# Performance work log

Measured on AMD Instinct MI355X. Metric: run time of the kernel, lower is better.

## Reference

```python
import jax, jax.numpy as jnp
import numpy as np

S, FEAT, D, H, L, DFF, C = 1024, 64, 512, 8, 2, 2048, 10
DB = D // 4  # distance-bias MLP hidden
NFREQ = D // 6  # 85 -> 6*85=510 dims, padded to 512
EPS = 1e-5


def _layernorm(x, g, b):
    mu = jnp.mean(x, axis=-1, keepdims=True)
    var = jnp.mean(jnp.square(x - mu), axis=-1, keepdims=True)
    return (x - mu) * jax.lax.rsqrt(var + EPS) * g + b


def setup_inputs() -> dict:
    key = jax.random.key(0)
    ks = iter(jax.random.split(key, 40))
    def w(shape, scale=0.02):
        return (jax.random.normal(next(ks), shape, jnp.float32) * scale)
    inp = {
        'features': jax.random.normal(next(ks), (S, FEAT), jnp.float32),
        'positions': jax.random.uniform(next(ks), (S, 3), jnp.float32),
        'freq_bands': jnp.asarray(10.0 ** np.linspace(0.0, 10.0, NFREQ), jnp.float32),
        'in_w': w((FEAT, D)), 'in_b': jnp.zeros((D,), jnp.float32),
        'qw': w((L, D, D)), 'qb': jnp.zeros((L, D), jnp.float32),
        'kw': w((L, D, D)), 'kb': jnp.zeros((L, D), jnp.float32),
        'vw': w((L, D, D)), 'vb': jnp.zeros((L, D), jnp.float32),
        'ow': w((L, D, D)), 'ob': jnp.zeros((L, D), jnp.float32),
        'db1w': w((L, 1, DB), 0.5), 'db1b': jnp.zeros((L, DB), jnp.float32),
        'db2w': w((L, DB, H), 0.1), 'db2b': jnp.zeros((L, H), jnp.float32),
        'n1g': jnp.ones((L, D), jnp.float32), 'n1b': jnp.zeros((L, D), jnp.float32),
        'n2g': jnp.ones((L, D), jnp.float32), 'n2b': jnp.zeros((L, D), jnp.float32),
        'f1w': w((L, D, DFF)), 'f1b': jnp.zeros((L, DFF), jnp.float32),
        'f2w': w((L, DFF, D)), 'f2b': jnp.zeros((L, D), jnp.float32),
        'c1w': w((D, D // 2)), 'c1b': jnp.zeros((D // 2,), jnp.float32),
        'c2w': w((D // 2, C)), 'c2b': jnp.zeros((C,), jnp.float32),
    }
    return inp


def _forward(features, positions, freq_bands, in_w, in_b, qw, qb, kw, kb, vw, vb,
             ow, ob, db1w, db1b, db2w, db2b, n1g, n1b, n2g, n2b,
             f1w, f1b, f2w, f2b, c1w, c1b, c2w, c2b):
    d_model = in_w.shape[1]
    nhead = db2w.shape[-1]
    head_dim = d_model // nhead
    scale = 1.0 / np.sqrt(head_dim)

    x = features[None] @ in_w + in_b            # [1, S, D]
    pos = positions[None]                        # [1, S, 3]

    # 3D sinusoidal positional encoding: [sin0,cos0,sin1,cos1,sin2,cos2]
    enc = []
    for i in range(3):
        cs = pos[..., i:i + 1] * freq_bands      # [1, S, NFREQ] (broadcast)
        enc.append(jnp.sin(cs))
        enc.append(jnp.cos(cs))
    pe = jnp.concatenate(enc, axis=-1)           # [1, S, 6*NFREQ]
    if pe.shape[-1] > d_model:
        pe = pe[..., :d_model]
    elif pe.shape[-1] < d_model:
        pe = jnp.pad(pe, ((0, 0), (0, 0), (0, d_model - pe.shape[-1])))
    x = x + pe

    # pairwise distances [1, S, S, 1]; safe sqrt (zero grad on diagonal)
    diff = pos[:, :, None, :] - pos[:, None, :, :]
    sq = jnp.sum(jnp.square(diff), axis=-1, keepdims=True)
    dist = jnp.sqrt(jnp.where(sq > 0, sq, 1.0)) * (sq > 0)

    n_layers = qw.shape[0]
    seq = x.shape[1]
    for l in range(n_layers):
        q = (x @ qw[l] + qb[l]).reshape(1, seq, nhead, head_dim)
        k = (x @ kw[l] + kb[l]).reshape(1, seq, nhead, head_dim)
        v = (x @ vw[l] + vb[l]).reshape(1, seq, nhead, head_dim)
        scores = jnp.einsum('bihd,bjhd->bhij', q, k) * scale  # [1,H,S,S]
        hbias = jax.nn.relu(dist @ db1w[l] + db1b[l])          # [1,S,S,DB]
        bias = jnp.einsum('bijc,ch->bhij', hbias, db2w[l]) + db2b[l][None, :, None, None]
        attn = jax.nn.softmax(scores + bias, axis=-1)
        out = jnp.einsum('bhij,bjhd->bihd', attn, v).reshape(1, seq, d_model)
        out = out @ ow[l] + ob[l]
        x = _layernorm(x + out, n1g[l], n1b[l])
        ffn = jax.nn.relu(x @ f1w[l] + f1b[l]) @ f2w[l] + f2b[l]
        x = _layernorm(x + ffn, n2g[l], n2b[l])

    pooled = jnp.mean(x, axis=1)                 # [1, D]
    return jax.nn.relu(pooled @ c1w + c1b) @ c2w + c2b  # [1, C]


def reference(features, positions, freq_bands, in_w, in_b, qw, qb, kw, kb, vw, vb,
              ow, ob, db1w, db1b, db2w, db2b, n1g, n1b, n2g, n2b,
              f1w, f1b, f2w, f2b, c1w, c1b, c2w, c2b):
    return _forward(features, positions, freq_bands, in_w, in_b, qw, qb, kw, kb, vw, vb,
                    ow, ob, db1w, db1b, db2w, db2b, n1g, n1b, n2g, n2b,
                    f1w, f1b, f2w, f2b, c1w, c1b, c2w, c2b)
```

## Files before the change

### kernel.cpp

```cpp
#include <hip/hip_runtime.h>

namespace {
constexpr int kS   = 1024;
constexpr int kD   = 512;
constexpr int kDFF = 2048;
constexpr int kNF  = 85;
}

typedef __attribute__((ext_vector_type(8))) short bhalf8_t;
typedef _Float16 half8_t __attribute__((ext_vector_type(8)));
typedef __attribute__((ext_vector_type(4))) float f32x4_t;

__device__ __forceinline__ float wave_sum(float v) {
#pragma unroll
    for (int o = 1; o < 64; o <<= 1) v += __shfl_xor(v, o, 64);
    return v;
}
__device__ __forceinline__ unsigned short f2h(float f) {
    _Float16 h = (_Float16)f;
    return __builtin_bit_cast(unsigned short, h);
}
__device__ __forceinline__ float h2f(unsigned short u) {
    return (float)__builtin_bit_cast(_Float16, u);
}

__global__ __launch_bounds__(256)
void prep_a_k(const float* __restrict__ feat, const float* __restrict__ pos,
              const float* __restrict__ fb, const float* __restrict__ in_w,
              const float* __restrict__ in_b, float* __restrict__ x,
              unsigned short* __restrict__ xb,
              float* __restrict__ dist,
              const float* __restrict__ a_, const float* __restrict__ b_,
              float* __restrict__ bp_out)
{
    __shared__ float smem[128];
    int bid = blockIdx.x;
    int t = threadIdx.x;
    if (bid < 1024) {
        int s = bid;
        if (t < 64) smem[t] = feat[s * 64 + t];
        __syncthreads();
        float acc0 = in_b[t], acc1 = in_b[t + 256];
#pragma unroll 8
        for (int c = 0; c < 64; ++c) {
            float fv = smem[c];
            acc0 = fmaf(fv, in_w[c * kD + t], acc0);
            acc1 = fmaf(fv, in_w[c * kD + 256 + t], acc1);
        }
        float pe0 = 0.f, pe1 = 0.f;
        {
            int d = t;
            if (d < 6 * kNF) {
                int seg = d / kNF, idx = d - seg * kNF;
                float cs = pos[s * 3 + (seg >> 1)] * fb[idx];
                pe0 = (seg & 1) ? cosf(cs) : sinf(cs);
            }
            d = t + 256;
            if (d < 6 * kNF) {
                int seg = d / kNF, idx = d - seg * kNF;
                float cs = pos[s * 3 + (seg >> 1)] * fb[idx];
                pe1 = (seg & 1) ? cosf(cs) : sinf(cs);
            }
        }
        float o0 = acc0 + pe0, o1 = acc1 + pe1;
        x[s * kD + t]        = o0;
        x[s * kD + 256 + t]  = o1;
        xb[s * kD + t]       = f2h(o0);
        xb[s * kD + 256 + t] = f2h(o1);
    } else if (bid < 2048) {
        int i = bid - 1024;
        float px = pos[i * 3], py = pos[i * 3 + 1], pz = pos[i * 3 + 2];
        for (int j = t; j < kS; j += 256) {
            float dx = px - pos[j * 3], dy = py - pos[j * 3 + 1], dz = pz - pos[j * 3 + 2];
            float sq = dx * dx + dy * dy + dz * dz;
            dist[(long)i * kS + j] = sq > 0.f ? sqrtf(sq) : 0.f;
        }
    } else {
        int l = bid - 2048;
        const float* ap = a_ + l * 128;
        const float* bp = b_ + l * 128;
        float* out = bp_out + l * 128;
        if (t < 128) {
            float a = ap[t], b = bp[t];
            smem[t] = (a != 0.f) ? (-b / a) : 3.0e38f;
        }
        __syncthreads();
        for (int ksz = 2; ksz <= 128; ksz <<= 1) {
            for (int j = ksz >> 1; j > 0; j >>= 1) {
                if (t < 128) {
                    int ixj = t ^ j;
                    if (ixj > t) {
                        bool up = ((t & ksz) == 0);
                        float x0 = smem[t], x1 = smem[ixj];
                        if ((x0 > x1) == up) { smem[t] = x1; smem[ixj] = x0; }
                    }
                }
                __syncthreads();
            }
        }
        if (t < 128) out[t] = smem[t];
    }
}

__device__ __forceinline__ void tr_tile32(const float* __restrict__ in,
                                          unsigned short* __restrict__ out,
                                          int N, int K, int k0, int n0, int t,
                                          float* tile )
{
    int r = t >> 3, c4 = (t & 7) * 4;
    float4 v = *reinterpret_cast<const float4*>(&in[(long)(k0 + r) * N + n0 + c4]);
    tile[r * 33 + c4] = v.x; tile[r * 33 + c4 + 1] = v.y;
    tile[r * 33 + c4 + 2] = v.z; tile[r * 33 + c4 + 3] = v.w;
    __syncthreads();
    int nr = t >> 3, kq = (t & 7) * 4;
    unsigned short h[4];
#pragma unroll
    for (int j = 0; j < 4; ++j) h[j] = f2h(tile[(kq + j) * 33 + nr]);
    *reinterpret_cast<ushort4*>(&out[(long)(n0 + nr) * K + k0 + kq]) =
        make_ushort4(h[0], h[1], h[2], h[3]);
}

__global__ __launch_bounds__(256)
void prep_w_k(const float* __restrict__ qw, const float* __restrict__ kw,
              const float* __restrict__ vw, const float* __restrict__ ow,
              unsigned short* __restrict__ qwb, unsigned short* __restrict__ kwb,
              unsigned short* __restrict__ vwb, unsigned short* __restrict__ owb,
              const float* __restrict__ f1w, unsigned short* __restrict__ f1wb,
              const float* __restrict__ f2w, unsigned short* __restrict__ f2wb,
              const float* __restrict__ a_, const float* __restrict__ b_,
              const float* __restrict__ w2, const float* __restrict__ b2,
              const float* __restrict__ bp, float* __restrict__ Atab,
              float* __restrict__ Btab)
{
    __shared__ float smem[32 * 33];
    int bid = blockIdx.x;
    int t = threadIdx.x;
    if (bid < 2048) {
        int zz = bid >> 8, rem = bid & 255;
        int mat = zz >> 1, layer = zz & 1;
        const float* in = (mat == 0) ? qw : (mat == 1) ? kw : (mat == 2) ? vw : ow;
        unsigned short* out = (mat == 0) ? qwb : (mat == 1) ? kwb : (mat == 2) ? vwb : owb;
        tr_tile32(in + (long)layer * 262144, out + (long)layer * 262144,
                  512, 512, (rem & 15) * 32, (rem >> 4) * 32, t, smem);
    } else if (bid < 4096) {
        int l = bid - 2048;
        int z = l >> 10;
        tr_tile32(f1w + (long)z * 1048576, f1wb + (long)z * 1048576,
                  2048, 512, (l & 15) * 32, ((l >> 4) & 63) * 32, t, smem);
    } else if (bid < 6144) {
        int l = bid - 4096;
        int z = l >> 10;
        tr_tile32(f2w + (long)z * 1048576, f2wb + (long)z * 1048576,
                  512, 2048, (l & 63) * 32, ((l >> 6) & 15) * 32, t, smem);
    } else {
        int l = bid - 6144;
        int seg = l % 129, ly = l / 129;
        const float* ap = a_ + ly * 128;
        const float* bpp = b_ + ly * 128;
        const float* w2p = w2 + ly * 1024;
        const float* b2p = b2 + ly * 8;
        const float* bpl = bp + ly * 128;
        float* At = Atab + ly * 1040;
        float* Bt = Btab + ly * 1040;

        float m;
        if (seg == 0)        m = bpl[0] - 1.0f;
        else if (seg == 128) m = bpl[127] + 1.0f;
        else                 m = 0.5f * (bpl[seg - 1] + bpl[seg]);

        int h = t & 7, cg = t >> 3;
        float A = 0.f, B = 0.f;
#pragma unroll
        for (int j = 0; j < 4; ++j) {
            int c = cg * 4 + j;
            float a = ap[c], b = bpp[c];
            if (fmaf(a, m, b) > 0.f) {
                float w = w2p[c * 8 + h];
                A = fmaf(a, w, A);
                B = fmaf(b, w, B);
            }
        }
#pragma unroll
        for (int off = 8; off < 64; off <<= 1) {
            A += __shfl_xor(A, off, 64);
            B += __shfl_xor(B, off, 64);
        }
        int w = t >> 6, lane = t & 63;
        if (lane < 8) { smem[w * 8 + lane] = A; smem[32 + w * 8 + lane] = B; }
        __syncthreads();
        if (t < 8) {
            float At_ = smem[t] + smem[8 + t] + smem[16 + t] + smem[24 + t];
            float Bt_ = smem[32 + t] + smem[40 + t] + smem[48 + t] + smem[56 + t];
            At[seg * 8 + t] = At_;
            Bt[seg * 8 + t] = Bt_ + b2p[t];
        }
    }
}

constexpr int BKp = 72;
constexpr int ASZ = 64 * BKp;
constexpr int BSZ = 128 * BKp;

template<int K>
__device__ __forceinline__ void gemm_core(
    const unsigned short* __restrict__ Ap, const unsigned short* __restrict__ Bp,
    int lda, int ldb, int bm, int bn, int tid,
    unsigned short* __restrict__ As, unsigned short* __restrict__ Bs,
    f32x4_t acc[2][4])
{
    int w = tid >> 6, lane = tid & 63, quad = lane >> 4, l16 = lane & 15;
    int wm = (w >> 1) * 32, wn = (w & 1) * 64;
    int ar = tid >> 2, ac = (tid & 3) * 16;
    int br = tid >> 1, bc = (tid & 1) * 32;
    const unsigned short* pa = Ap + (long)(bm + ar) * lda + ac;
    const unsigned short* pb = Bp + (long)(bn + br) * ldb + bc;

    bhalf8_t a0_0, a0_1, b0_0, b0_1, b0_2, b0_3;
    bhalf8_t a1_0, a1_1, b1_0, b1_1, b1_2, b1_3;

#define LDG(S, k0) do { \
    a##S##_0 = *reinterpret_cast<const bhalf8_t*>(pa + (k0)); \
    a##S##_1 = *reinterpret_cast<const bhalf8_t*>(pa + (k0) + 8); \
    b##S##_0 = *reinterpret_cast<const bhalf8_t*>(pb + (k0)); \
    b##S##_1 = *reinterpret_cast<const bhalf8_t*>(pb + (k0) + 8); \
    b##S##_2 = *reinterpret_cast<const bhalf8_t*>(pb + (k0) + 16); \
    b##S##_3 = *reinterpret_cast<const bhalf8_t*>(pb + (k0) + 24); } while (0)
#define STG(S, as, bs) do { \
    *reinterpret_cast<bhalf8_t*>(&(as)[ar * BKp + ac])      = a##S##_0; \
    *reinterpret_cast<bhalf8_t*>(&(as)[ar * BKp + ac + 8])  = a##S##_1; \
    *reinterpret_cast<bhalf8_t*>(&(bs)[br * BKp + bc])      = b##S##_0; \
    *reinterpret_cast<bhalf8_t*>(&(bs)[br * BKp + bc + 8])  = b##S##_1; \
    *reinterpret_cast<bhalf8_t*>(&(bs)[br * BKp + bc + 16]) = b##S##_2; \
    *reinterpret_cast<bhalf8_t*>(&(bs)[br * BKp + bc + 24]) = b##S##_3; } while (0)

    constexpr int NT = K / 64;
    LDG(0, 0);
    STG(0, As, Bs);
    if (NT > 1) LDG(1, 64);
#pragma unroll
    for (int t = 0; t < NT; ++t) {
        __syncthreads();
        if (t + 2 < NT) {
            if ((t & 1) == 0) LDG(0, (t + 2) * 64);
            else              LDG(1, (t + 2) * 64);
        }
        const unsigned short* as = As + (t & 1) * ASZ;
        const unsigned short* bs = Bs + (t & 1) * BSZ;
#pragma unroll
        for (int kq = 0; kq < 2; ++kq) {
            bhalf8_t af[2], bf[4];
#pragma unroll
            for (int i = 0; i < 2; ++i)
                af[i] = *reinterpret_cast<const bhalf8_t*>(
                    &as[(wm + i * 16 + l16) * BKp + kq * 32 + quad * 8]);
#pragma unroll
            for (int j = 0; j < 4; ++j)
                bf[j] = *reinterpret_cast<const bhalf8_t*>(
                    &bs[(wn + j * 16 + l16) * BKp + kq * 32 + quad * 8]);
#pragma unroll
            for (int i = 0; i < 2; ++i)
#pragma unroll
                for (int j = 0; j < 4; ++j)
                    acc[i][j] = __builtin_amdgcn_mfma_f32_16x16x32_f16(
                        __builtin_bit_cast(half8_t, af[i]), __builtin_bit_cast(half8_t, bf[j]),
                        acc[i][j], 0, 0, 0);
        }
        if (t + 1 < NT) {
            if (((t + 1) & 1) == 0) STG(0, As, Bs);
            else                    STG(1, As + ASZ, Bs + BSZ);
        }
    }
#undef LDG
#undef STG
}

__global__ __launch_bounds__(256, 2)
void qkv_bias_k(const unsigned short* __restrict__ xb,
                const unsigned short* __restrict__ qwb, const unsigned short* __restrict__ kwb,
                const unsigned short* __restrict__ vwb,
                const float* __restrict__ qbias, const float* __restrict__ kbias,
                const float* __restrict__ vbias,
                unsigned short* __restrict__ qb2, unsigned short* __restrict__ kb2,
                unsigned short* __restrict__ vtb,
                const float* __restrict__ dist, const float* __restrict__ bp,
                const float* __restrict__ Atab, const float* __restrict__ Btab,
                unsigned short* __restrict__ bmap, unsigned int* __restrict__ cnt)
{
    __shared__ __align__(16) unsigned short smem[2 * ASZ + 2 * BSZ];
    int bid = blockIdx.x;
    int tid = threadIdx.x;
    if (bid < 192) {
        int z = bid >> 6, rem = bid & 63;
        int bm = (rem & 15) * 64, bn = (rem >> 4) * 128;
        const unsigned short* Bp = (z == 1) ? kwb : (z == 2) ? vwb : qwb;
        const float* bias = (z == 1) ? kbias : (z == 2) ? vbias : qbias;
        f32x4_t acc[2][4] = {};
        gemm_core<512>(xb, Bp, 512, 512, bm, bn, tid, smem, smem + 2 * ASZ, acc);

        int w = tid >> 6, lane = tid & 63, quad = lane >> 4, l16 = lane & 15;
        int wm = (w >> 1) * 32, wn = (w & 1) * 64;
        if (z == 2) {
            __syncthreads();
            unsigned short* T = smem;
#pragma unroll
            for (int j = 0; j < 4; ++j) {
                int ln = wn + j * 16 + l16;
                float bv = bias[bn + ln];
#pragma unroll
                for (int i = 0; i < 2; ++i)
#pragma unroll
                    for (int r = 0; r < 4; ++r)
                        T[ln * BKp + wm + i * 16 + quad * 4 + r] =
                            f2h((acc[i][j][r] + bv) * 1024.f);
            }
            __syncthreads();
            int nr = tid >> 1, mc = (tid & 1) * 32;
            int gn = bn + nr;
            unsigned short* dst = vtb + (long)(gn >> 6) * 65536
                                + (long)(gn & 63) * 1024 + bm + mc;
#pragma unroll
            for (int jj = 0; jj < 4; ++jj)
                *reinterpret_cast<bhalf8_t*>(dst + jj * 8) =
                    *reinterpret_cast<const bhalf8_t*>(&T[nr * BKp + mc + jj * 8]);
        } else {
#pragma unroll
            for (int j = 0; j < 4; ++j) {
                int n = bn + wn + j * 16 + l16;
                float bv = bias[n];
                unsigned short* dst = ((z == 1) ? kb2 : qb2)
                    + (long)(n >> 6) * 131072 + (n & 63);
#pragma unroll
                for (int i = 0; i < 2; ++i)
#pragma unroll
                    for (int r = 0; r < 4; ++r) {
                        int m = bm + wm + i * 16 + quad * 4 + r;
                        float s = acc[i][j][r] + bv;
                        unsigned short hi = f2h(s);
                        dst[(long)m * 128]      = hi;
                        dst[(long)m * 128 + 64] = (z == 0) ? f2h(s - h2f(hi)) : hi;
                    }
            }
        }
    } else {
        if (bid == 192 && tid < 8) cnt[tid] = 0;
        float* fs = reinterpret_cast<float*>(smem);
        float* bps = fs;
        float* Ah  = fs + 128;
        float* Bh  = fs + 1160;
        int t = tid;
        if (t < 128) bps[t] = bp[t];
        for (int i = t; i < 1032; i += 256) { Ah[i] = Atab[i]; Bh[i] = Btab[i]; }
        __syncthreads();
        long i = ((long)(bid - 192) * 256 + t) * 4;
        float4 d4 = *reinterpret_cast<const float4*>(dist + i);
        float dv[4] = {d4.x, d4.y, d4.z, d4.w};
        int seg[4];
#pragma unroll
        for (int j = 0; j < 4; ++j) {
            float tv = dv[j];
            int lo = 0, hi = 128;
            while (lo < hi) { int mid = (lo + hi) >> 1; if (bps[mid] < tv) lo = mid + 1; else hi = mid; }
            seg[j] = lo;
        }
        long gm  = i >> 10;
        int gn0  = (int)(i & 1023);
        int zz   = gn0 >> 7, nb = (gn0 >> 4) & 7, c4 = gn0 & 15;
        long pbase = gm * 1024 + zz * 128 + nb;
#pragma unroll
        for (int h = 0; h < 8; ++h) {
            unsigned short* bh = bmap + (long)h * 1048576 + pbase;
#pragma unroll
            for (int j = 0; j < 4; ++j)
                bh[(c4 + j) * 8] =
                    f2h(fmaf(Ah[seg[j] * 8 + h], dv[j], Bh[seg[j] * 8 + h]));
        }
    }
}

__global__ __launch_bounds__(256, 2)
void bgemm_ffn1_k(const unsigned short* __restrict__ A,
                  const unsigned short* __restrict__ B,
                  const float* __restrict__ bias,
                  unsigned short* __restrict__ hb)
{
    __shared__ __align__(16) unsigned short smem[2 * ASZ + 2 * BSZ];
    int tid = threadIdx.x;
    int bm = blockIdx.x * 64, bn = blockIdx.y * 128;
    f32x4_t acc[2][4] = {};
    gemm_core<512>(A, B, 512, 512, bm, bn, tid, smem, smem + 2 * ASZ, acc);

    int w = tid >> 6, lane = tid & 63, quad = lane >> 4, l16 = lane & 15;
    int wm = (w >> 1) * 32, wn = (w & 1) * 64;
#pragma unroll
    for (int j = 0; j < 4; ++j) {
        int n = bn + wn + j * 16 + l16;
        float bv = bias[n];
#pragma unroll
        for (int i = 0; i < 2; ++i)
#pragma unroll
            for (int r = 0; r < 4; ++r) {
                int m = bm + wm + i * 16 + quad * 4 + r;
                hb[(long)m * kDFF + n] = f2h(fmaxf(acc[i][j][r] + bv, 0.f));
            }
    }
}

template<int K>
__global__ __launch_bounds__(256, 2)
void bgemm_k(const unsigned short* __restrict__ A, const unsigned short* __restrict__ B,
             int N, int lda, int ldb, unsigned short* __restrict__ Cpart)
{
    __shared__ __align__(16) unsigned short smem[2 * ASZ + 2 * BSZ];
    int tid = threadIdx.x;
    int ks = blockIdx.z;
    const unsigned short* Ap = A + (long)ks * K;
    const unsigned short* Bp = B + (long)ks * K;
    int bm = blockIdx.x * 64, bn = blockIdx.y * 128;
    f32x4_t acc[2][4] = {};
    gemm_core<K>(Ap, Bp, lda, ldb, bm, bn, tid, smem, smem + 2 * ASZ, acc);

    int w = tid >> 6, lane = tid & 63, quad = lane >> 4, l16 = lane & 15;
    int wm = (w >> 1) * 32, wn = (w & 1) * 64;
    unsigned short* Cp = Cpart + (long)ks * kS * N;
#pragma unroll
    for (int i = 0; i < 2; ++i)
#pragma unroll
        for (int j = 0; j < 4; ++j)
#pragma unroll
            for (int r = 0; r < 4; ++r) {
                int m = bm + wm + i * 16 + quad * 4 + r;
                int n = bn + wn + j * 16 + l16;
                Cp[(long)m * N + n] = f2h(acc[i][j][r]);
            }
}

__global__ __launch_bounds__(256, 3)
void flash_part_k(const unsigned short* __restrict__ qb2, const unsigned short* __restrict__ kb2,
                  const unsigned short* __restrict__ vtb, const unsigned short* __restrict__ bmap,
                  unsigned short* __restrict__ po, float* __restrict__ pm, float* __restrict__ pl)
{
    constexpr int KP = 136;
    __shared__ __align__(16) unsigned short Klds[128 * KP];
    __shared__ __align__(16) unsigned short Vlds[64 * KP];

    int tid = threadIdx.x;
    int w    = tid >> 6;
    int lane = tid & 63;
    int quad = lane >> 4, l16 = lane & 15;

    int wg  = blockIdx.x;
    int lin = (wg & 7) * 128 + (wg >> 3);
    int qbg = lin & 15;
    int h   = (lin >> 4) & 7;
    int z   = lin >> 7;
    int qb  = qbg * 4 + w;
    int bm  = qb * 16;
    int k0  = z * 128;

    const unsigned short* Qh = qb2 + (long)h * 131072;
    const unsigned short* Kh = kb2 + (long)h * 131072;
    const unsigned short* Vh = vtb + (long)h * 65536;
    const unsigned short* Bm = bmap + (long)h * 1048576;

    {
        int kr = tid >> 1, kc = (tid & 1) * 64;
#pragma unroll
        for (int j = 0; j < 8; ++j)
            *reinterpret_cast<bhalf8_t*>(&Klds[kr * KP + kc + j * 8]) =
                *reinterpret_cast<const bhalf8_t*>(&Kh[(long)(k0 + kr) * 128 + kc + j * 8]);
        int vr = tid >> 2, vc = (tid & 3) * 32;
#pragma unroll
        for (int j = 0; j < 4; ++j)
            *reinterpret_cast<bhalf8_t*>(&Vlds[vr * KP + vc + j * 8]) =
                *reinterpret_cast<const bhalf8_t*>(&Vh[(long)vr * 1024 + k0 + vc + j * 8]);
    }

    bhalf8_t aq[4];
#pragma unroll
    for (int kq = 0; kq < 4; ++kq)
        aq[kq] = *reinterpret_cast<const bhalf8_t*>(
            &Qh[(long)(bm + l16) * 128 + kq * 32 + quad * 8]);
    bhalf8_t bias8[4];
#pragma unroll
    for (int r = 0; r < 4; ++r) {
        int gm = bm + quad * 4 + r;
        bias8[r] = *reinterpret_cast<const bhalf8_t*>(
            &Bm[(long)gm * 1024 + z * 128 + l16 * 8]);
    }

    __syncthreads();

    f32x4_t sacc[8] = {};
#pragma unroll
    for (int kq = 0; kq < 4; ++kq) {
        bhalf8_t bk[8];
#pragma unroll
        for (int nb = 0; nb < 8; ++nb)
            bk[nb] = *reinterpret_cast<const bhalf8_t*>(
                &Klds[(nb * 16 + l16) * KP + kq * 32 + quad * 8]);
#pragma unroll
        for (int nb = 0; nb < 8; ++nb)
            sacc[nb] = __builtin_amdgcn_mfma_f32_16x16x32_f16(
                __builtin_bit_cast(half8_t, aq[kq]), __builtin_bit_cast(half8_t, bk[nb]),
                sacc[nb], 0, 0, 0);
    }

    float m_r[4] = {-3.0e38f, -3.0e38f, -3.0e38f, -3.0e38f};
#pragma unroll
    for (int nb = 0; nb < 8; ++nb)
#pragma unroll
        for (int r = 0; r < 4; ++r) {
            float bias = h2f((unsigned short)bias8[r][nb]);
            float s = fmaf(sacc[nb][r], 0.125f, bias);
            sacc[nb][r] = s;
            m_r[r] = fmaxf(m_r[r], s);
        }
#pragma unroll
    for (int r = 0; r < 4; ++r) {
        float m_ = m_r[r];
#pragma unroll
        for (int off = 1; off < 16; off <<= 1) m_ = fmaxf(m_, __shfl_xor(m_, off, 64));
        m_r[r] = m_;
    }

    __syncthreads();

    unsigned short* Ps = Klds + w * 16 * KP;
    float l_r[4];
#pragma unroll
    for (int r = 0; r < 4; ++r) {
        int row = quad * 4 + r;
        float mN = m_r[r];
        float s_ = 0.f;
#pragma unroll
        for (int nb = 0; nb < 8; ++nb) {
            float p = __expf(sacc[nb][r] - mN);
            Ps[row * KP + nb * 16 + l16] = f2h(p * 16384.f);
            s_ += p;
        }
#pragma unroll
        for (int off = 1; off < 16; off <<= 1) s_ += __shfl_xor(s_, off, 64);
        l_r[r] = s_;
    }

    long sbase = (((long)z * 8 + h) * 64 + qb) * 16;
    if (l16 == 0) {
#pragma unroll
        for (int r = 0; r < 4; ++r) {
            pm[sbase + quad * 4 + r] = m_r[r];
            pl[sbase + quad * 4 + r] = l_r[r];
        }
    }

    f32x4_t oacc[4] = {};
#pragma unroll
    for (int kq2 = 0; kq2 < 4; ++kq2) {
        bhalf8_t ap = *reinterpret_cast<const bhalf8_t*>(&Ps[l16 * KP + kq2 * 32 + quad * 8]);
#pragma unroll
        for (int j2 = 0; j2 < 4; ++j2) {
            bhalf8_t bv = *reinterpret_cast<const bhalf8_t*>(
                &Vlds[(j2 * 16 + l16) * KP + kq2 * 32 + quad * 8]);
            oacc[j2] = __builtin_amdgcn_mfma_f32_16x16x32_f16(
                __builtin_bit_cast(half8_t, ap), __builtin_bit_cast(half8_t, bv),
                oacc[j2], 0, 0, 0);
        }
    }

    unsigned short* pob = po + sbase * 64;
#pragma unroll
    for (int j2 = 0; j2 < 4; ++j2)
#pragma unroll
        for (int r = 0; r < 4; ++r)
            pob[(quad * 4 + r) * 64 + j2 * 16 + l16] =
                f2h(oacc[j2][r] * (1.f / 16777216.f));
}

__global__ __launch_bounds__(256)
void flash_merge_k(const unsigned short* __restrict__ po, const float* __restrict__ pm,
                   const float* __restrict__ pl, unsigned short* __restrict__ aob)
{
    int t = blockIdx.x * 256 + threadIdx.x;
    int c8  = t & 7;
    int row = (t >> 3) & 15;
    int qb  = (t >> 7) & 63;
    int h   = t >> 13;
    long sidx = (((long)h * 64) + qb) * 16 + row;

    float m[8];
    float M = -3.0e38f;
#pragma unroll
    for (int z = 0; z < 8; ++z) { m[z] = pm[z * 8192 + sidx]; M = fmaxf(M, m[z]); }
    float w[8], lt = 0.f;
#pragma unroll
    for (int z = 0; z < 8; ++z) {
        w[z] = __expf(m[z] - M);
        lt = fmaf(pl[z * 8192 + sidx], w[z], lt);
    }
    float acc[8] = {};
#pragma unroll
    for (int z = 0; z < 8; ++z) {
        const unsigned short* p = po + (z * 8192 + sidx) * 64 + c8 * 8;
        ushort4 a = *reinterpret_cast<const ushort4*>(p);
        ushort4 b = *reinterpret_cast<const ushort4*>(p + 4);
        acc[0] = fmaf(h2f(a.x), w[z], acc[0]); acc[1] = fmaf(h2f(a.y), w[z], acc[1]);
        acc[2] = fmaf(h2f(a.z), w[z], acc[2]); acc[3] = fmaf(h2f(a.w), w[z], acc[3]);
        acc[4] = fmaf(h2f(b.x), w[z], acc[4]); acc[5] = fmaf(h2f(b.y), w[z], acc[5]);
        acc[6] = fmaf(h2f(b.z), w[z], acc[6]); acc[7] = fmaf(h2f(b.w), w[z], acc[7]);
    }
    float inv = 1.f / lt;
    unsigned short hi[8];
#pragma unroll
    for (int j = 0; j < 8; ++j) hi[j] = f2h(acc[j] * inv);
    long base = ((long)qb * 16 + row) * 512 + h * 64 + c8 * 8;
    *reinterpret_cast<ushort4*>(&aob[base])     = make_ushort4(hi[0], hi[1], hi[2], hi[3]);
    *reinterpret_cast<ushort4*>(&aob[base + 4]) = make_ushort4(hi[4], hi[5], hi[6], hi[7]);
}

__global__ __launch_bounds__(256)
void add_ln_fused_k(const unsigned short* __restrict__ part, float* __restrict__ x,
                    const float* __restrict__ bias,
                    const float* __restrict__ g, const float* __restrict__ b,
                    unsigned short* __restrict__ xb, int splitk)
{
    __shared__ float sm[4];
    int row = blockIdx.x, t = threadIdx.x;
    const long MN = (long)kS * kD;
    float* xr = x + (long)row * kD;
    float s0 = 0.f, s1 = 0.f;
    const unsigned short* pr = part + (long)row * kD;
    for (int sl = 0; sl < splitk; ++sl) {
        s0 += h2f(pr[(long)sl * MN + t]);
        s1 += h2f(pr[(long)sl * MN + t + 256]);
    }
    s0 += bias[t] + xr[t];
    s1 += bias[t + 256] + xr[t + 256];
    float sum = wave_sum(s0 + s1);
    if ((t & 63) == 0) sm[t >> 6] = sum;
    __syncthreads();
    sum = sm[0] + sm[1] + sm[2] + sm[3];
    float mu = sum * (1.f / kD);
    float d0 = s0 - mu, d1 = s1 - mu;
    __syncthreads();
    float vs = wave_sum(d0 * d0 + d1 * d1);
    if ((t & 63) == 0) sm[t >> 6] = vs;
    __syncthreads();
    vs = sm[0] + sm[1] + sm[2] + sm[3];
    float rs = rsqrtf(vs * (1.f / kD) + 1e-5f);
    float o0 = fmaf(d0 * rs, g[t], b[t]);
    float o1 = fmaf(d1 * rs, g[t + 256], b[t + 256]);
    xr[t]       = o0;
    xr[t + 256] = o1;
    unsigned short* xrow = xb + (long)row * 512;
    xrow[t]       = f2h(o0);
    xrow[t + 256] = f2h(o1);
}

__global__ __launch_bounds__(256)
void pool_head_k(const float* __restrict__ x, float* __restrict__ partial,
                 unsigned int* __restrict__ cnt2,
                 const float* __restrict__ c1w, const float* __restrict__ c1b,
                 const float* __restrict__ c2w, const float* __restrict__ c2b,
                 float* __restrict__ out)
{
    __shared__ float pooled[kD];
    __shared__ float h1[256];
    __shared__ int isLast;
    int t = threadIdx.x;
    int cb = blockIdx.x & 1, rb = blockIdx.x >> 1;
    int col = cb * 256 + t;
    float s = 0.f;
    for (int r = rb * 128; r < rb * 128 + 128; ++r) s += x[(long)r * kD + col];
    partial[rb * kD + col] = s;

    __threadfence();
    if (t == 0) isLast = (atomicAdd(cnt2, 1u) == 15u);
    __syncthreads();
    if (!isLast) return;
    __threadfence();

    for (int d = t; d < kD; d += 256) {
        float ps = 0.f;
        for (int r = 0; r < 8; ++r) ps += partial[r * kD + d];
        pooled[d] = ps * (1.0f / kS);
    }
    __syncthreads();
    float acc = c1b[t];
    for (int f = 0; f < kD; ++f) acc = fmaf(pooled[f], c1w[f * 256 + t], acc);
    h1[t] = fmaxf(acc, 0.f);
    __syncthreads();
    if (t < 10) {
        float o = c2b[t];
        for (int f = 0; f < 256; ++f) o = fmaf(h1[f], c2w[f * 10 + t], o);
        out[t] = o;
    }
}

extern "C" void kernel_launch(void* const* d_in, const int* in_sizes, int n_in,
                              void* d_out, int out_size, void* d_ws, size_t ws_size,
                              hipStream_t stream)
{
    (void)in_sizes; (void)n_in; (void)out_size; (void)ws_size;
    const float* features = (const float*)d_in[0];
    const float* positions= (const float*)d_in[1];
    const float* fb       = (const float*)d_in[2];
    const float* in_w     = (const float*)d_in[3];
    const float* in_b     = (const float*)d_in[4];
    const float* qw  = (const float*)d_in[5];
    const float* qb  = (const float*)d_in[6];
    const float* kw  = (const float*)d_in[7];
    const float* kb  = (const float*)d_in[8];
    const float* vw  = (const float*)d_in[9];
    const float* vb  = (const float*)d_in[10];
    const float* ow  = (const float*)d_in[11];
    const float* ob  = (const float*)d_in[12];
    const float* db1w= (const float*)d_in[13];
    const float* db1b= (const float*)d_in[14];
    const float* db2w= (const float*)d_in[15];
    const float* db2b= (const float*)d_in[16];
    const float* n1g = (const float*)d_in[17];
    const float* n1b = (const float*)d_in[18];
    const float* n2g = (const float*)d_in[19];
    const float* n2b = (const float*)d_in[20];
    const float* f1w = (const float*)d_in[21];
    const float* f1b = (const float*)d_in[22];
    const float* f2w = (const float*)d_in[23];
    const float* f2b = (const float*)d_in[24];
    const float* c1w = (const float*)d_in[25];
    const float* c1b = (const float*)d_in[26];
    const float* c2w = (const float*)d_in[27];
    const float* c2b = (const float*)d_in[28];

    float* ws = (float*)d_ws;
    const long SD = (long)kS * kD;
    float* x      = ws;
    float* dist   = ws + 3 * SD;
    float* part_f = ws + 5 * SD;
    float* bpw    = ws + 17 * SD;
    float* Atab   = bpw + 256;
    float* Btab   = Atab + 2080;
    float* partial= Btab + 2080;

    unsigned short* part16 = (unsigned short*)part_f;
    unsigned short* po     = (unsigned short*)part_f;
    float* pmv = part_f + 4194304 / 2 + 65536;
    float* plv = pmv + 65536;
    unsigned int* cnt2 = (unsigned int*)(plv + 65536);

    unsigned short* ub = (unsigned short*)(ws + 17 * SD + 8512);
    unsigned short* xb   = ub;
    unsigned short* aob  = xb   + 524288;
    unsigned short* qb2  = aob  + 524288;
    unsigned short* kb2  = qb2  + 1048576;
    unsigned short* vtb  = kb2  + 1048576;
    unsigned short* hb   = vtb  + 524288;
    unsigned short* qwb  = hb   + 2097152;
    unsigned short* kwb  = qwb  + 524288;
    unsigned short* vwb  = kwb  + 524288;
    unsigned short* owb  = vwb  + 524288;
    unsigned short* f1wb = owb  + 524288;
    unsigned short* f2wb = f1wb + 2097152;
    unsigned short* bmap = f2wb + 2097152;

    prep_a_k<<<2050, 256, 0, stream>>>(features, positions, fb, in_w, in_b, x, xb,
                                       dist, db1w, db1b, bpw);
    prep_w_k<<<6402, 256, 0, stream>>>(qw, kw, vw, ow, qwb, kwb, vwb, owb,
                                       f1w, f1wb, f2w, f2wb,
                                       db1w, db1b, db2w, db2b, bpw, Atab, Btab);

    for (int l = 0; l < 2; ++l) {
        qkv_bias_k<<<1216, 256, 0, stream>>>(
            xb, qwb + l * 262144, kwb + l * 262144, vwb + l * 262144,
            qb + l * kD, kb + l * kD, vb + l * kD, qb2, kb2, vtb,
            dist, bpw + l * 128, Atab + l * 1040, Btab + l * 1040, bmap, cnt2);

        flash_part_k<<<1024, 256, 0, stream>>>(
            qb2, kb2, vtb, bmap, po, pmv, plv);
        flash_merge_k<<<256, 256, 0, stream>>>(po, pmv, plv, aob);

        bgemm_k<128><<<dim3(16, 4, 4), 256, 0, stream>>>(
            aob, owb + l * 262144, 512, 512, 512, part16);
        add_ln_fused_k<<<kS, 256, 0, stream>>>(
            part16, x, ob + l * kD, n1g + l * kD, n1b + l * kD, xb, 4);

        bgemm_ffn1_k<<<dim3(16, 16), 256, 0, stream>>>(
            xb, f1wb + l * 1048576, f1b + l * kDFF, hb);

        bgemm_k<512><<<dim3(16, 4, 4), 256, 0, stream>>>(
            hb, f2wb + l * 1048576, 512, 2048, 2048, part16);
        add_ln_fused_k<<<kS, 256, 0, stream>>>(
            part16, x, f2b + l * kD, n2g + l * kD, n2b + l * kD, xb, 4);
    }

    pool_head_k<<<16, 256, 0, stream>>>(x, partial, cnt2, c1w, c1b, c2w, c2b,
                                        (float*)d_out);
}
```

Baseline: 289.6 us.

## Fuse flash-merge into output-projection GEMM and merge prep kernels

Removes the separate flash_merge kernel by merging split-KV partial outputs (max/sum rescaling) directly into the A-tile load of a new output-projection GEMM, so the merged attention output never round-trips through global memory. The two prep kernels are combined into one launch, the input projection processes four rows per block, and the breakpoint sort is recomputed per Atab block instead of waiting on a prior kernel. The extra launches and the aob buffer go away, at the cost of redundant merge work per N-tile (the merge is repeated for each of 4 column blocks) and repeated sorting in each table block.

```diff
diff --git a/kernel.cpp b/kernel.cpp
--- a/kernel.cpp
+++ b/kernel.cpp
@@ -24,31 +24,62 @@
     return (float)__builtin_bit_cast(_Float16, u);
 }
 
+__device__ __forceinline__ void tr_tile32(const float* __restrict__ in,
+                                          unsigned short* __restrict__ out,
+                                          int N, int K, int k0, int n0, int t,
+                                          float* tile )
+{
+    int r = t >> 3, c4 = (t & 7) * 4;
+    float4 v = *reinterpret_cast<const float4*>(&in[(long)(k0 + r) * N + n0 + c4]);
+    tile[r * 33 + c4] = v.x; tile[r * 33 + c4 + 1] = v.y;
+    tile[r * 33 + c4 + 2] = v.z; tile[r * 33 + c4 + 3] = v.w;
+    __syncthreads();
+    int nr = t >> 3, kq = (t & 7) * 4;
+    unsigned short h[4];
+#pragma unroll
+    for (int j = 0; j < 4; ++j) h[j] = f2h(tile[(kq + j) * 33 + nr]);
+    *reinterpret_cast<ushort4*>(&out[(long)(n0 + nr) * K + k0 + kq]) =
+        make_ushort4(h[0], h[1], h[2], h[3]);
+}
+
 __global__ __launch_bounds__(256)
-void prep_a_k(const float* __restrict__ feat, const float* __restrict__ pos,
-              const float* __restrict__ fb, const float* __restrict__ in_w,
-              const float* __restrict__ in_b, float* __restrict__ x,
-              unsigned short* __restrict__ xb,
-              float* __restrict__ dist,
-              const float* __restrict__ a_, const float* __restrict__ b_,
-              float* __restrict__ bp_out)
-{
-    __shared__ float smem[128];
+void prep_k(const float* __restrict__ feat, const float* __restrict__ pos,
+            const float* __restrict__ fb, const float* __restrict__ in_w,
+            const float* __restrict__ in_b, float* __restrict__ x,
+            unsigned short* __restrict__ xb, float* __restrict__ dist,
+            const float* __restrict__ qw, const float* __restrict__ kw,
+            const float* __restrict__ vw, const float* __restrict__ ow,
+            unsigned short* __restrict__ qwb, unsigned short* __restrict__ kwb,
+            unsigned short* __restrict__ vwb, unsigned short* __restrict__ owb,
+            const float* __restrict__ f1w, unsigned short* __restrict__ f1wb,
+            const float* __restrict__ f2w, unsigned short* __restrict__ f2wb,
+            const float* __restrict__ a_, const float* __restrict__ b_,
+            const float* __restrict__ w2, const float* __restrict__ b2,
+            float* __restrict__ bp_out, float* __restrict__ Atab,
+            float* __restrict__ Btab)
+{
+    __shared__ float smem[1056];
     int bid = blockIdx.x;
     int t = threadIdx.x;
-    if (bid < 1024) {
-        int s = bid;
-        if (t < 64) smem[t] = feat[s * 64 + t];
+    if (bid < 256) {
+        int s0 = bid * 4;
+        smem[t] = feat[s0 * 64 + t];
         __syncthreads();
-        float acc0 = in_b[t], acc1 = in_b[t + 256];
-#pragma unroll 8
+        float b0 = in_b[t], b1 = in_b[t + 256];
+        float a0[4] = {b0, b0, b0, b0}, a1[4] = {b1, b1, b1, b1};
+#pragma unroll 4
         for (int c = 0; c < 64; ++c) {
-            float fv = smem[c];
-            acc0 = fmaf(fv, in_w[c * kD + t], acc0);
-            acc1 = fmaf(fv, in_w[c * kD + 256 + t], acc1);
-        }
-        float pe0 = 0.f, pe1 = 0.f;
-        {
+            float w0 = in_w[c * kD + t], w1 = in_w[c * kD + 256 + t];
+#pragma unroll
+            for (int r = 0; r < 4; ++r) {
+                a0[r] = fmaf(smem[r * 64 + c], w0, a0[r]);
+                a1[r] = fmaf(smem[r * 64 + c], w1, a1[r]);
+            }
+        }
+#pragma unroll
+        for (int r = 0; r < 4; ++r) {
+            int s = s0 + r;
+            float pe0 = 0.f, pe1 = 0.f;
             int d = t;
             if (d < 6 * kNF) {
                 int seg = d / kNF, idx = d - seg * kNF;
@@ -61,27 +92,52 @@
                 float cs = pos[s * 3 + (seg >> 1)] * fb[idx];
                 pe1 = (seg & 1) ? cosf(cs) : sinf(cs);
             }
-        }
-        float o0 = acc0 + pe0, o1 = acc1 + pe1;
-        x[s * kD + t]        = o0;
-        x[s * kD + 256 + t]  = o1;
-        xb[s * kD + t]       = f2h(o0);
-        xb[s * kD + 256 + t] = f2h(o1);
-    } else if (bid < 2048) {
-        int i = bid - 1024;
+            float o0 = a0[r] + pe0, o1 = a1[r] + pe1;
+            x[s * kD + t]        = o0;
+            x[s * kD + 256 + t]  = o1;
+            xb[s * kD + t]       = f2h(o0);
+            xb[s * kD + 256 + t] = f2h(o1);
+        }
+    } else if (bid < 1280) {
+        int i = bid - 256;
         float px = pos[i * 3], py = pos[i * 3 + 1], pz = pos[i * 3 + 2];
         for (int j = t; j < kS; j += 256) {
             float dx = px - pos[j * 3], dy = py - pos[j * 3 + 1], dz = pz - pos[j * 3 + 2];
             float sq = dx * dx + dy * dy + dz * dz;
             dist[(long)i * kS + j] = sq > 0.f ? sqrtf(sq) : 0.f;
         }
+    } else if (bid < 7424) {
+        int idx = bid - 1280;
+        if (idx < 2048) {
+            int zz = idx >> 8, rem = idx & 255;
+            int mat = zz >> 1, layer = zz & 1;
+            const float* in = (mat == 0) ? qw : (mat == 1) ? kw : (mat == 2) ? vw : ow;
+            unsigned short* out = (mat == 0) ? qwb : (mat == 1) ? kwb : (mat == 2) ? vwb : owb;
+            tr_tile32(in + (long)layer * 262144, out + (long)layer * 262144,
+                      512, 512, (rem & 15) * 32, (rem >> 4) * 32, t, smem);
+        } else if (idx < 4096) {
+            int l = idx - 2048;
+            int z = l >> 10;
+            tr_tile32(f1w + (long)z * 1048576, f1wb + (long)z * 1048576,
+                      2048, 512, (l & 15) * 32, ((l >> 4) & 63) * 32, t, smem);
+        } else {
+            int l = idx - 4096;
+            int z = l >> 10;
+            tr_tile32(f2w + (long)z * 1048576, f2wb + (long)z * 1048576,
+                      512, 2048, (l & 63) * 32, ((l >> 6) & 15) * 32, t, smem);
+        }
     } else {
-        int l = bid - 2048;
-        const float* ap = a_ + l * 128;
-        const float* bp = b_ + l * 128;
-        float* out = bp_out + l * 128;
+        int l = bid - 7424;
+        int seg = l % 129, ly = l / 129;
+        const float* ap = a_ + ly * 128;
+        const float* bpp = b_ + ly * 128;
+        const float* w2p = w2 + ly * 1024;
+        const float* b2p = b2 + ly * 8;
+        float* At = Atab + ly * 1040;
+        float* Bt = Btab + ly * 1040;
+
         if (t < 128) {
-            float a = ap[t], b = bp[t];
+            float a = ap[t], b = bpp[t];
             smem[t] = (a != 0.f) ? (-b / a) : 3.0e38f;
         }
         __syncthreads();
@@ -98,75 +154,12 @@
                 __syncthreads();
             }
         }
-        if (t < 128) out[t] = smem[t];
-    }
-}
-
-__device__ __forceinline__ void tr_tile32(const float* __restrict__ in,
-                                          unsigned short* __restrict__ out,
-                                          int N, int K, int k0, int n0, int t,
-                                          float* tile )
-{
-    int r = t >> 3, c4 = (t & 7) * 4;
-    float4 v = *reinterpret_cast<const float4*>(&in[(long)(k0 + r) * N + n0 + c4]);
-    tile[r * 33 + c4] = v.x; tile[r * 33 + c4 + 1] = v.y;
-    tile[r * 33 + c4 + 2] = v.z; tile[r * 33 + c4 + 3] = v.w;
-    __syncthreads();
-    int nr = t >> 3, kq = (t & 7) * 4;
-    unsigned short h[4];
-#pragma unroll
-    for (int j = 0; j < 4; ++j) h[j] = f2h(tile[(kq + j) * 33 + nr]);
-    *reinterpret_cast<ushort4*>(&out[(long)(n0 + nr) * K + k0 + kq]) =
-        make_ushort4(h[0], h[1], h[2], h[3]);
-}
-
-__global__ __launch_bounds__(256)
-void prep_w_k(const float* __restrict__ qw, const float* __restrict__ kw,
-              const float* __restrict__ vw, const float* __restrict__ ow,
-              unsigned short* __restrict__ qwb, unsigned short* __restrict__ kwb,
-              unsigned short* __restrict__ vwb, unsigned short* __restrict__ owb,
-              const float* __restrict__ f1w, unsigned short* __restrict__ f1wb,
-              const float* __restrict__ f2w, unsigned short* __restrict__ f2wb,
-              const float* __restrict__ a_, const float* __restrict__ b_,
-              const float* __restrict__ w2, const float* __restrict__ b2,
-              const float* __restrict__ bp, float* __restrict__ Atab,
-              float* __restrict__ Btab)
-{
-    __shared__ float smem[32 * 33];
-    int bid = blockIdx.x;
-    int t = threadIdx.x;
-    if (bid < 2048) {
-        int zz = bid >> 8, rem = bid & 255;
-        int mat = zz >> 1, layer = zz & 1;
-        const float* in = (mat == 0) ? qw : (mat == 1) ? kw : (mat == 2) ? vw : ow;
-        unsigned short* out = (mat == 0) ? qwb : (mat == 1) ? kwb : (mat == 2) ? vwb : owb;
-        tr_tile32(in + (long)layer * 262144, out + (long)layer * 262144,
-                  512, 512, (rem & 15) * 32, (rem >> 4) * 32, t, smem);
-    } else if (bid < 4096) {
-        int l = bid - 2048;
-        int z = l >> 10;
-        tr_tile32(f1w + (long)z * 1048576, f1wb + (long)z * 1048576,
-                  2048, 512, (l & 15) * 32, ((l >> 4) & 63) * 32, t, smem);
-    } else if (bid < 6144) {
-        int l = bid - 4096;
-        int z = l >> 10;
-        tr_tile32(f2w + (long)z * 1048576, f2wb + (long)z * 1048576,
-                  512, 2048, (l & 63) * 32, ((l >> 6) & 15) * 32, t, smem);
-    } else {
-        int l = bid - 6144;
-        int seg = l % 129, ly = l / 129;
-        const float* ap = a_ + ly * 128;
-        const float* bpp = b_ + ly * 128;
-        const float* w2p = w2 + ly * 1024;
-        const float* b2p = b2 + ly * 8;
-        const float* bpl = bp + ly * 128;
-        float* At = Atab + ly * 1040;
-        float* Bt = Btab + ly * 1040;
-
         float m;
-        if (seg == 0)        m = bpl[0] - 1.0f;
-        else if (seg == 128) m = bpl[127] + 1.0f;
-        else                 m = 0.5f * (bpl[seg - 1] + bpl[seg]);
+        if (seg == 0)        m = smem[0] - 1.0f;
+        else if (seg == 128) m = smem[127] + 1.0f;
+        else                 m = 0.5f * (smem[seg - 1] + smem[seg]);
+        if (seg == 0 && t < 128) bp_out[ly * 128 + t] = smem[t];
+        __syncthreads();
 
         int h = t & 7, cg = t >> 3;
         float A = 0.f, B = 0.f;
@@ -434,6 +427,121 @@
             }
 }
 
+__global__ __launch_bounds__(256, 2)
+void bgemm_oproj_k(const unsigned short* __restrict__ po,
+                   const float* __restrict__ pm, const float* __restrict__ pl,
+                   const unsigned short* __restrict__ Bw,
+                   unsigned short* __restrict__ Cpart)
+{
+    __shared__ __align__(16) unsigned short As[2 * ASZ];
+    __shared__ __align__(16) unsigned short Bs[2 * BSZ];
+    __shared__ float wz_s[2][64][9];
+    __shared__ float inv_s[2][64];
+
+    int tid = threadIdx.x;
+    int ks = blockIdx.z;
+    int bm = blockIdx.x * 64, bn = blockIdx.y * 128;
+    int h0 = ks * 2;
+
+    int br = tid >> 1, bc = (tid & 1) * 32;
+    {
+        const unsigned short* pb = Bw + (long)(bn + br) * 512 + ks * 128 + bc;
+#pragma unroll
+        for (int t = 0; t < 2; ++t) {
+            bhalf8_t v0 = *reinterpret_cast<const bhalf8_t*>(pb + t * 64);
+            bhalf8_t v1 = *reinterpret_cast<const bhalf8_t*>(pb + t * 64 + 8);
+            bhalf8_t v2 = *reinterpret_cast<const bhalf8_t*>(pb + t * 64 + 16);
+            bhalf8_t v3 = *reinterpret_cast<const bhalf8_t*>(pb + t * 64 + 24);
+            unsigned short* bs = Bs + t * BSZ;
+            *reinterpret_cast<bhalf8_t*>(&bs[br * BKp + bc])      = v0;
+            *reinterpret_cast<bhalf8_t*>(&bs[br * BKp + bc + 8])  = v1;
+            *reinterpret_cast<bhalf8_t*>(&bs[br * BKp + bc + 16]) = v2;
+            *reinterpret_cast<bhalf8_t*>(&bs[br * BKp + bc + 24]) = v3;
+        }
+    }
+
+    if (tid < 128) {
+        int t = tid >> 6, r = tid & 63;
+        long sidx = (long)(h0 + t) * 1024 + bm + r;
+        float m[8], M = -3.0e38f;
+#pragma unroll
+        for (int z = 0; z < 8; ++z) { m[z] = pm[z * 8192 + sidx]; M = fmaxf(M, m[z]); }
+        float lt = 0.f;
+#pragma unroll
+        for (int z = 0; z < 8; ++z) {
+            float w = __expf(m[z] - M);
+            wz_s[t][r][z] = w;
+            lt = fmaf(pl[z * 8192 + sidx], w, lt);
+        }
+        inv_s[t][r] = 1.f / lt;
+    }
+    __syncthreads();
+
+    int ar = tid >> 2, ac = (tid & 3) * 16;
+#pragma unroll
+    for (int t = 0; t < 2; ++t) {
+        float inv = inv_s[t][ar];
+        const unsigned short* p = po + ((long)(h0 + t) * 1024 + bm + ar) * 64 + ac;
+        float acc[16] = {};
+#pragma unroll
+        for (int z = 0; z < 8; ++z) {
+            float w = wz_s[t][ar][z];
+            bhalf8_t v0 = *reinterpret_cast<const bhalf8_t*>(p + (long)z * 524288);
+            bhalf8_t v1 = *reinterpret_cast<const bhalf8_t*>(p + (long)z * 524288 + 8);
+#pragma unroll
+            for (int j = 0; j < 8; ++j) {
+                acc[j]     = fmaf(h2f((unsigned short)v0[j]), w, acc[j]);
+                acc[8 + j] = fmaf(h2f((unsigned short)v1[j]), w, acc[8 + j]);
+            }
+        }
+        unsigned short* as = As + t * ASZ;
+#pragma unroll
+        for (int j = 0; j < 16; ++j)
+            as[ar * BKp + ac + j] = f2h(acc[j] * inv);
+    }
+    __syncthreads();
+
+    int w = tid >> 6, lane = tid & 63, quad = lane >> 4, l16 = lane & 15;
+    int wm = (w >> 1) * 32, wn = (w & 1) * 64;
+    f32x4_t accf[2][4] = {};
+#pragma unroll
+    for (int t = 0; t < 2; ++t) {
+        const unsigned short* as = As + t * ASZ;
+        const unsigned short* bs = Bs + t * BSZ;
+#pragma unroll
+        for (int kq = 0; kq < 2; ++kq) {
+            bhalf8_t af[2], bf[4];
+#pragma unroll
+            for (int i = 0; i < 2; ++i)
+                af[i] = *reinterpret_cast<const bhalf8_t*>(
+                    &as[(wm + i * 16 + l16) * BKp + kq * 32 + quad * 8]);
+#pragma unroll
+            for (int j = 0; j < 4; ++j)
+                bf[j] = *reinterpret_cast<const bhalf8_t*>(
+                    &bs[(wn + j * 16 + l16) * BKp + kq * 32 + quad * 8]);
+#pragma unroll
+            for (int i = 0; i < 2; ++i)
+#pragma unroll
+                for (int j = 0; j < 4; ++j)
+                    accf[i][j] = __builtin_amdgcn_mfma_f32_16x16x32_f16(
+                        __builtin_bit_cast(half8_t, af[i]), __builtin_bit_cast(half8_t, bf[j]),
+                        accf[i][j], 0, 0, 0);
+        }
+    }
+
+    unsigned short* Cp = Cpart + (long)ks * kS * 512;
+#pragma unroll
+    for (int i = 0; i < 2; ++i)
+#pragma unroll
+        for (int j = 0; j < 4; ++j)
+#pragma unroll
+            for (int r = 0; r < 4; ++r) {
+                int m = bm + wm + i * 16 + quad * 4 + r;
+                int n = bn + wn + j * 16 + l16;
+                Cp[(long)m * 512 + n] = f2h(accf[i][j][r]);
+            }
+}
+
 __global__ __launch_bounds__(256, 3)
 void flash_part_k(const unsigned short* __restrict__ qb2, const unsigned short* __restrict__ kb2,
                   const unsigned short* __restrict__ vtb, const unsigned short* __restrict__ bmap,
@@ -573,47 +681,6 @@
         for (int r = 0; r < 4; ++r)
             pob[(quad * 4 + r) * 64 + j2 * 16 + l16] =
                 f2h(oacc[j2][r] * (1.f / 16777216.f));
-}
-
-__global__ __launch_bounds__(256)
-void flash_merge_k(const unsigned short* __restrict__ po, const float* __restrict__ pm,
-                   const float* __restrict__ pl, unsigned short* __restrict__ aob)
-{
-    int t = blockIdx.x * 256 + threadIdx.x;
-    int c8  = t & 7;
-    int row = (t >> 3) & 15;
-    int qb  = (t >> 7) & 63;
-    int h   = t >> 13;
-    long sidx = (((long)h * 64) + qb) * 16 + row;
-
-    float m[8];
-    float M = -3.0e38f;
-#pragma unroll
-    for (int z = 0; z < 8; ++z) { m[z] = pm[z * 8192 + sidx]; M = fmaxf(M, m[z]); }
-    float w[8], lt = 0.f;
-#pragma unroll
-    for (int z = 0; z < 8; ++z) {
-        w[z] = __expf(m[z] - M);
-        lt = fmaf(pl[z * 8192 + sidx], w[z], lt);
-    }
-    float acc[8] = {};
-#pragma unroll
-    for (int z = 0; z < 8; ++z) {
-        const unsigned short* p = po + (z * 8192 + sidx) * 64 + c8 * 8;
-        ushort4 a = *reinterpret_cast<const ushort4*>(p);
-        ushort4 b = *reinterpret_cast<const ushort4*>(p + 4);
-        acc[0] = fmaf(h2f(a.x), w[z], acc[0]); acc[1] = fmaf(h2f(a.y), w[z], acc[1]);
-        acc[2] = fmaf(h2f(a.z), w[z], acc[2]); acc[3] = fmaf(h2f(a.w), w[z], acc[3]);
-        acc[4] = fmaf(h2f(b.x), w[z], acc[4]); acc[5] = fmaf(h2f(b.y), w[z], acc[5]);
-        acc[6] = fmaf(h2f(b.z), w[z], acc[6]); acc[7] = fmaf(h2f(b.w), w[z], acc[7]);
-    }
-    float inv = 1.f / lt;
-    unsigned short hi[8];
-#pragma unroll
-    for (int j = 0; j < 8; ++j) hi[j] = f2h(acc[j] * inv);
-    long base = ((long)qb * 16 + row) * 512 + h * 64 + c8 * 8;
-    *reinterpret_cast<ushort4*>(&aob[base])     = make_ushort4(hi[0], hi[1], hi[2], hi[3]);
-    *reinterpret_cast<ushort4*>(&aob[base + 4]) = make_ushort4(hi[4], hi[5], hi[6], hi[7]);
 }
 
 __global__ __launch_bounds__(256)
@@ -742,14 +809,14 @@
 
     unsigned short* part16 = (unsigned short*)part_f;
     unsigned short* po     = (unsigned short*)part_f;
-    float* pmv = part_f + 4194304 / 2 + 65536;
+    float* pmv = part_f + 2162688;
     float* plv = pmv + 65536;
     unsigned int* cnt2 = (unsigned int*)(plv + 65536);
+    unsigned short* part16b = (unsigned short*)(part_f + 2293792);
 
     unsigned short* ub = (unsigned short*)(ws + 17 * SD + 8512);
     unsigned short* xb   = ub;
-    unsigned short* aob  = xb   + 524288;
-    unsigned short* qb2  = aob  + 524288;
+    unsigned short* qb2  = ub   + 1048576;
     unsigned short* kb2  = qb2  + 1048576;
     unsigned short* vtb  = kb2  + 1048576;
     unsigned short* hb   = vtb  + 524288;
@@ -761,11 +828,10 @@
     unsigned short* f2wb = f1wb + 2097152;
     unsigned short* bmap = f2wb + 2097152;
 
-    prep_a_k<<<2050, 256, 0, stream>>>(features, positions, fb, in_w, in_b, x, xb,
-                                       dist, db1w, db1b, bpw);
-    prep_w_k<<<6402, 256, 0, stream>>>(qw, kw, vw, ow, qwb, kwb, vwb, owb,
-                                       f1w, f1wb, f2w, f2wb,
-                                       db1w, db1b, db2w, db2b, bpw, Atab, Btab);
+    prep_k<<<7682, 256, 0, stream>>>(features, positions, fb, in_w, in_b, x, xb,
+                                     dist, qw, kw, vw, ow, qwb, kwb, vwb, owb,
+                                     f1w, f1wb, f2w, f2wb,
+                                     db1w, db1b, db2w, db2b, bpw, Atab, Btab);
 
     for (int l = 0; l < 2; ++l) {
         qkv_bias_k<<<1216, 256, 0, stream>>>(
@@ -775,12 +841,11 @@
 
         flash_part_k<<<1024, 256, 0, stream>>>(
             qb2, kb2, vtb, bmap, po, pmv, plv);
-        flash_merge_k<<<256, 256, 0, stream>>>(po, pmv, plv, aob);
-
-        bgemm_k<128><<<dim3(16, 4, 4), 256, 0, stream>>>(
-            aob, owb + l * 262144, 512, 512, 512, part16);
+
+        bgemm_oproj_k<<<dim3(16, 4, 4), 256, 0, stream>>>(
+            po, pmv, plv, owb + l * 262144, part16b);
         add_ln_fused_k<<<kS, 256, 0, stream>>>(
-            part16, x, ob + l * kD, n1g + l * kD, n1b + l * kD, xb, 4);
+            part16b, x, ob + l * kD, n1g + l * kD, n1b + l * kD, xb, 4);
 
         bgemm_ffn1_k<<<dim3(16, 16), 256, 0, stream>>>(
             xb, f1wb + l * 1048576, f1b + l * kDFF, hb);
```

After: 279.8 us. 1.03x faster.
